# Kernel optimization log

Measured on AMD Instinct MI355X. Metric: run time of the kernel, lower is better.

Reference implementation:

```python
import jax, jax.numpy as jnp
import numpy as np

IN, OUT, TOKENS = 4096, 11008, 32

def setup_inputs() -> dict:
    key = jax.random.key(0)
    k1, k2, k3, k4 = jax.random.split(key, 4)
    x = jax.random.normal(k1, (TOKENS, IN), dtype=jnp.float16)
    # symmetric int8 quantized weights in [-127, 127]
    weight_q = jax.random.randint(k2, (OUT, IN), -127, 128, dtype=jnp.int8)
    # per-output-channel scales, positive, shape [OUT, 1]
    scale = (jax.random.uniform(k3, (OUT, 1), dtype=jnp.float32) * 0.01 + 1e-4).astype(jnp.float16)
    bias = jax.random.normal(k4, (OUT,), dtype=jnp.float16)
    return {"x": x, "weight_q": weight_q, "scale": scale, "bias": bias}

def reference(x, weight_q, scale, bias):
    # weight_fp[o, i] = weight_q[o, i] * scale[o, 0]  (fp16 dequant on the fly)
    weight_deq = weight_q.astype(scale.dtype) * scale  # [OUT, IN] fp16
    # F.linear: y = x @ W^T + b
    return jnp.einsum('ti,oi->to', x, weight_deq) + bias
```

## Files before the change

### kernel.cpp

```cpp
#include <hip/hip_runtime.h>
#include <hip/hip_bf16.h>

#define IN_F  4096
#define OUT_F 11008

typedef _Float16 half8 __attribute__((ext_vector_type(8)));
typedef _Float16 half4 __attribute__((ext_vector_type(4)));
typedef __fp16   fp16x2 __attribute__((ext_vector_type(2)));
typedef float    f32x4 __attribute__((ext_vector_type(4)));
typedef int      i32x4 __attribute__((ext_vector_type(4)));

__global__ __launch_bounds__(512, 4)
void dql_fused(const float* __restrict__ x,
               const int* __restrict__ wq,
               const float* __restrict__ scale,
               const float* __restrict__ bias,
               float* __restrict__ out)
{
    __shared__ __align__(16) _Float16 wlds[8][16][72];
    __shared__ __align__(16) _Float16 xlds[8][32][72];
    __shared__ float red[8][64][9];

    const int tid  = threadIdx.x;
    const int wid  = tid >> 6;
    const int lane = tid & 63;
    const int c    = lane & 15;
    const int kg   = lane >> 4;
    const int srow = lane >> 2;
    const int scol = (lane & 3) * 4;
    const int xr   = lane >> 3;
    const int xc   = (lane & 7) * 4;
    const int obase = blockIdx.x * 16;
    const int kbase = wid * 512;

    const int* wrow = wq + (size_t)(obase + srow) * IN_F + kbase + scol;
    const float* xb0 = x + (size_t)xr * IN_F + kbase + xc;

    f32x4 acc0 = {0.f, 0.f, 0.f, 0.f};
    f32x4 acc1 = {0.f, 0.f, 0.f, 0.f};

    i32x4 w0[4], w1[4];
    f32x4 xh0[4], xh1[4];

    auto LOADW = [&](i32x4* wbuf, int ch) {
        #pragma unroll
        for (int i = 0; i < 4; ++i)
            wbuf[i] = *(const i32x4*)(wrow + ch * 64 + i * 16);
    };
    auto LOADXH = [&](f32x4* xbuf, int ch, int sub) {
        #pragma unroll
        for (int q2 = 0; q2 < 4; ++q2)
            xbuf[q2] = *(const f32x4*)(xb0 + (size_t)q2 * 8 * IN_F + ch * 64 + sub * 32);
    };
    auto STAGEW = [&](i32x4* wbuf) {
        #pragma unroll
        for (int i = 0; i < 4; ++i) {
            union { fp16x2 v2[2]; half4 v4; } u;
            u.v2[0] = __builtin_amdgcn_cvt_pkrtz((float)wbuf[i][0], (float)wbuf[i][1]);
            u.v2[1] = __builtin_amdgcn_cvt_pkrtz((float)wbuf[i][2], (float)wbuf[i][3]);
            *(half4*)&wlds[wid][srow][scol + i * 16] = u.v4;
        }
    };
    auto STAGEXH = [&](f32x4* xbuf, int sub) {
        #pragma unroll
        for (int q2 = 0; q2 < 4; ++q2) {
            union { fp16x2 v2[2]; half4 v4; } u;
            u.v2[0] = __builtin_amdgcn_cvt_pkrtz(xbuf[q2][0], xbuf[q2][1]);
            u.v2[1] = __builtin_amdgcn_cvt_pkrtz(xbuf[q2][2], xbuf[q2][3]);
            *(half4*)&xlds[wid][q2 * 8 + xr][sub * 32 + xc] = u.v4;
        }
    };
    auto COMPUTE = [&](int sub) {
        half8 wf  = *(half8*)&wlds[wid][c][sub * 32 + kg * 8];
        half8 xf0 = *(half8*)&xlds[wid][c][sub * 32 + kg * 8];
        half8 xf1 = *(half8*)&xlds[wid][16 + c][sub * 32 + kg * 8];
        acc0 = __builtin_amdgcn_mfma_f32_16x16x32_f16(xf0, wf, acc0, 0, 0, 0);
        acc1 = __builtin_amdgcn_mfma_f32_16x16x32_f16(xf1, wf, acc1, 0, 0, 0);
    };

    LOADW(w0, 0); LOADW(w1, 1);
    LOADXH(xh0, 0, 0);

    #pragma unroll
    for (int ch = 0; ch < 8; ++ch) {
        i32x4* wcur = (ch & 1) ? w1 : w0;
        STAGEW(wcur);
        LOADXH(xh1, ch, 1);
        STAGEXH(xh0, 0);
        COMPUTE(0);
        if (ch + 1 < 8) LOADXH(xh0, ch + 1, 0);
        STAGEXH(xh1, 1);
        COMPUTE(1);
        if (ch + 2 < 8) LOADW(wcur, ch + 2);
    }

    #pragma unroll
    for (int r = 0; r < 4; ++r) {
        red[wid][lane][r]     = acc0[r];
        red[wid][lane][4 + r] = acc1[r];
    }
    __syncthreads();

    const int rlane = tid & 63;
    const int slot  = tid >> 6;
    float s = 0.f;
    #pragma unroll
    for (int wv = 0; wv < 8; ++wv) s += red[wv][rlane][slot];

    const int h = slot >> 2;
    const int r = slot & 3;
    const int t = h * 16 + (rlane >> 4) * 4 + r;
    const int o = obase + (rlane & 15);

    out[t * OUT_F + o] = s * scale[o] + bias[o];
}

extern "C" void kernel_launch(void* const* d_in, const int* in_sizes, int n_in,
                              void* d_out, int out_size, void* d_ws, size_t ws_size,
                              hipStream_t stream) {
    const float* x     = (const float*)d_in[0];
    const int*   wq    = (const int*)d_in[1];
    const float* scale = (const float*)d_in[2];
    const float* bias  = (const float*)d_in[3];
    float*       out   = (float*)d_out;

    dql_fused<<<OUT_F / 16, 512, 0, stream>>>(x, wq, scale, bias, out);
}
```

Measured before the change: 34.67 us.

## Shrink LDS footprint and registers to raise occupancy to six blocks

```diff
diff --git a/kernel.cpp b/kernel.cpp
--- a/kernel.cpp
+++ b/kernel.cpp
@@ -3,6 +3,10 @@
 
 #define IN_F  4096
 #define OUT_F 11008
+#define WSTR  68
+#define WV_W  (16 * WSTR * 2)
+#define WV_X  (32 * WSTR * 2)
+#define WV_BYTES (WV_W + WV_X)
 
 typedef _Float16 half8 __attribute__((ext_vector_type(8)));
 typedef _Float16 half4 __attribute__((ext_vector_type(4)));
@@ -10,16 +14,14 @@
 typedef float    f32x4 __attribute__((ext_vector_type(4)));
 typedef int      i32x4 __attribute__((ext_vector_type(4)));
 
-__global__ __launch_bounds__(512, 4)
+__global__ __launch_bounds__(512, 6)
 void dql_fused(const float* __restrict__ x,
                const int* __restrict__ wq,
                const float* __restrict__ scale,
                const float* __restrict__ bias,
                float* __restrict__ out)
 {
-    __shared__ __align__(16) _Float16 wlds[8][16][72];
-    __shared__ __align__(16) _Float16 xlds[8][32][72];
-    __shared__ float red[8][64][9];
+    __shared__ __align__(16) unsigned char smem[8][WV_BYTES];
 
     const int tid  = threadIdx.x;
     const int wid  = tid >> 6;
@@ -33,6 +35,9 @@
     const int obase = blockIdx.x * 16;
     const int kbase = wid * 512;
 
+    _Float16* wlds = (_Float16*)(&smem[wid][0]);
+    _Float16* xlds = (_Float16*)(&smem[wid][WV_W]);
+
     const int* wrow = wq + (size_t)(obase + srow) * IN_F + kbase + scol;
     const float* xb0 = x + (size_t)xr * IN_F + kbase + xc;
 
@@ -40,17 +45,17 @@
     f32x4 acc1 = {0.f, 0.f, 0.f, 0.f};
 
     i32x4 w0[4], w1[4];
-    f32x4 xh0[4], xh1[4];
+    f32x4 xh[4];
 
     auto LOADW = [&](i32x4* wbuf, int ch) {
         #pragma unroll
         for (int i = 0; i < 4; ++i)
             wbuf[i] = *(const i32x4*)(wrow + ch * 64 + i * 16);
     };
-    auto LOADXH = [&](f32x4* xbuf, int ch, int sub) {
+    auto LOADXH = [&](int ch, int sub) {
         #pragma unroll
         for (int q2 = 0; q2 < 4; ++q2)
-            xbuf[q2] = *(const f32x4*)(xb0 + (size_t)q2 * 8 * IN_F + ch * 64 + sub * 32);
+            xh[q2] = *(const f32x4*)(xb0 + (size_t)q2 * 8 * IN_F + ch * 64 + sub * 32);
     };
     auto STAGEW = [&](i32x4* wbuf) {
         #pragma unroll
@@ -58,46 +63,42 @@
             union { fp16x2 v2[2]; half4 v4; } u;
             u.v2[0] = __builtin_amdgcn_cvt_pkrtz((float)wbuf[i][0], (float)wbuf[i][1]);
             u.v2[1] = __builtin_amdgcn_cvt_pkrtz((float)wbuf[i][2], (float)wbuf[i][3]);
-            *(half4*)&wlds[wid][srow][scol + i * 16] = u.v4;
+            *(half4*)&wlds[srow * WSTR + scol + i * 16] = u.v4;
         }
     };
-    auto STAGEXH = [&](f32x4* xbuf, int sub) {
+    auto STAGEXH = [&](int sub) {
         #pragma unroll
         for (int q2 = 0; q2 < 4; ++q2) {
             union { fp16x2 v2[2]; half4 v4; } u;
-            u.v2[0] = __builtin_amdgcn_cvt_pkrtz(xbuf[q2][0], xbuf[q2][1]);
-            u.v2[1] = __builtin_amdgcn_cvt_pkrtz(xbuf[q2][2], xbuf[q2][3]);
-            *(half4*)&xlds[wid][q2 * 8 + xr][sub * 32 + xc] = u.v4;
+            u.v2[0] = __builtin_amdgcn_cvt_pkrtz(xh[q2][0], xh[q2][1]);
+            u.v2[1] = __builtin_amdgcn_cvt_pkrtz(xh[q2][2], xh[q2][3]);
+            *(half4*)&xlds[(q2 * 8 + xr) * WSTR + sub * 32 + xc] = u.v4;
         }
     };
     auto COMPUTE = [&](int sub) {
-        half8 wf  = *(half8*)&wlds[wid][c][sub * 32 + kg * 8];
-        half8 xf0 = *(half8*)&xlds[wid][c][sub * 32 + kg * 8];
-        half8 xf1 = *(half8*)&xlds[wid][16 + c][sub * 32 + kg * 8];
+        half8 wf  = *(half8*)&wlds[c * WSTR + sub * 32 + kg * 8];
+        half8 xf0 = *(half8*)&xlds[c * WSTR + sub * 32 + kg * 8];
+        half8 xf1 = *(half8*)&xlds[(16 + c) * WSTR + sub * 32 + kg * 8];
         acc0 = __builtin_amdgcn_mfma_f32_16x16x32_f16(xf0, wf, acc0, 0, 0, 0);
         acc1 = __builtin_amdgcn_mfma_f32_16x16x32_f16(xf1, wf, acc1, 0, 0, 0);
     };
 
     LOADW(w0, 0); LOADW(w1, 1);
-    LOADXH(xh0, 0, 0);
 
     #pragma unroll
     for (int ch = 0; ch < 8; ++ch) {
         i32x4* wcur = (ch & 1) ? w1 : w0;
         STAGEW(wcur);
-        LOADXH(xh1, ch, 1);
-        STAGEXH(xh0, 0);
-        COMPUTE(0);
-        if (ch + 1 < 8) LOADXH(xh0, ch + 1, 0);
-        STAGEXH(xh1, 1);
-        COMPUTE(1);
+        LOADXH(ch, 0); STAGEXH(0); COMPUTE(0);
+        LOADXH(ch, 1); STAGEXH(1); COMPUTE(1);
         if (ch + 2 < 8) LOADW(wcur, ch + 2);
     }
 
+    float* redw = (float*)(&smem[wid][WV_W]);
     #pragma unroll
     for (int r = 0; r < 4; ++r) {
-        red[wid][lane][r]     = acc0[r];
-        red[wid][lane][4 + r] = acc1[r];
+        redw[lane * 9 + r]     = acc0[r];
+        redw[lane * 9 + 4 + r] = acc1[r];
     }
     __syncthreads();
 
@@ -105,7 +106,8 @@
     const int slot  = tid >> 6;
     float s = 0.f;
     #pragma unroll
-    for (int wv = 0; wv < 8; ++wv) s += red[wv][rlane][slot];
+    for (int wv = 0; wv < 8; ++wv)
+        s += ((const float*)(&smem[wv][WV_W]))[rlane * 9 + slot];
 
     const int h = slot >> 2;
     const int r = slot & 3;
```

New measurement: 52.76 us. 1.52x slower.
